# Performance work log

Measured on AMD Instinct MI355X. Metric: run time of the kernel, lower is better.

The kernel has to match this reference:

```python
import jax, jax.numpy as jnp
import numpy as np

N_HEAD = 8
N_FEAT = 512
D_HEAD = N_FEAT // N_HEAD


def setup_inputs() -> dict:
    key = jax.random.key(0)
    ks = jax.random.split(key, 11)
    B, T, L = 4, 2048, 16
    s = 1.0 / np.sqrt(D_HEAD)
    so = 1.0 / np.sqrt(N_FEAT)
    return {
        "q": jax.random.normal(ks[0], (B, T, 1, N_FEAT), jnp.float32),
        "k": jax.random.normal(ks[1], (B, T, L, N_FEAT), jnp.float32),
        "v": jax.random.normal(ks[2], (B, T, L, N_FEAT), jnp.float32),
        "Wq": jax.random.uniform(ks[3], (D_HEAD, D_HEAD), jnp.float32, -s, s),
        "bq": jax.random.uniform(ks[4], (D_HEAD,), jnp.float32, -s, s),
        "Wk": jax.random.uniform(ks[5], (D_HEAD, D_HEAD), jnp.float32, -s, s),
        "bk": jax.random.uniform(ks[6], (D_HEAD,), jnp.float32, -s, s),
        "Wv": jax.random.uniform(ks[7], (D_HEAD, D_HEAD), jnp.float32, -s, s),
        "bv": jax.random.uniform(ks[8], (D_HEAD,), jnp.float32, -s, s),
        "Wo": jax.random.uniform(ks[9], (N_FEAT, N_FEAT), jnp.float32, -so, so),
        "bo": jax.random.uniform(ks[10], (N_FEAT,), jnp.float32, -so, so),
    }


def reference(q, k, v, Wq, bq, Wk, bk, Wv, bv, Wo, bo):
    B, T, L, F = k.shape
    H, D = N_HEAD, D_HEAD
    # split heads: q [B,T,H,D] (query axis of length 1 squeezed), k/v [B,T,L,H,D]
    qh = q.reshape(B, T, H, D)
    kh = k.reshape(B, T, L, H, D)
    vh = v.reshape(B, T, L, H, D)
    # per-head linear projections (shared across heads), Linear: x @ W^T + b
    qh = jnp.einsum("bthd,ed->bthe", qh, Wq) + bq
    kh = jnp.einsum("btlhd,ed->btlhe", kh, Wk) + bk
    vh = jnp.einsum("btlhd,ed->btlhe", vh, Wv) + bv
    # attention scores over the local window L (query length 1 per timestep)
    attw = jnp.einsum("bthd,btlhd->bthl", qh, kh) / jnp.sqrt(jnp.asarray(D, qh.dtype))
    attn = jax.nn.softmax(attw, axis=-1)  # dropout is identity in eval mode
    ct = jnp.einsum("bthl,btlhd->bthd", attn, vh)
    ct = ct.reshape(B, T, F)
    return ct @ Wo.T + bo
```

## Files before the change

### kernel.cpp

```cpp
#include <hip/hip_runtime.h>


#define NFEAT 512
#define NHEAD 8
#define DHEAD 64
#define LWIN  16
#define WPOS  8
#define NBT   4

typedef __attribute__((ext_vector_type(8))) short bf16x8;
typedef __attribute__((ext_vector_type(4))) float f32x4;

__device__ __forceinline__ unsigned short f2bf(float f) {
    unsigned int u = __float_as_uint(f);
    unsigned int r = (u + 0x7fffu + ((u >> 16) & 1u)) >> 16;
    return (unsigned short)r;
}

__global__ void precompute_small(const float* __restrict__ Wq, const float* __restrict__ bq,
                                 const float* __restrict__ Wk,
                                 const float* __restrict__ Wo, const float* __restrict__ bo,
                                 const float* __restrict__ bv,
                                 float* __restrict__ A, float* __restrict__ g,
                                 float* __restrict__ b2) {
    int idx = blockIdx.x * 256 + threadIdx.x;
    if (idx < 4096) {
        int d = idx >> 6, dp = idx & 63;
        float s = 0.f;
        #pragma unroll 8
        for (int e = 0; e < 64; ++e) s = fmaf(Wq[e * 64 + d], Wk[e * 64 + dp], s);
        A[idx] = s;
    } else if (idx < 4160) {
        int dp = idx - 4096;
        float s = 0.f;
        #pragma unroll 8
        for (int e = 0; e < 64; ++e) s = fmaf(Wk[e * 64 + dp], bq[e], s);
        g[dp] = s;
    } else if (idx < 4672) {
        int j = idx - 4160;
        float s = bo[j];
        #pragma unroll 8
        for (int i = 0; i < 512; ++i) s = fmaf(Wo[j * 512 + i], bv[i & 63], s);
        b2[j] = s;
    }
}

__global__ void precompute_wo2(const float* __restrict__ Wo, const float* __restrict__ Wv,
                               unsigned short* __restrict__ Wo2B) {
    int idx = blockIdx.x * 256 + threadIdx.x;
    int i = idx & 511, j = idx >> 9;
    int h = i >> 6, e = i & 63;
    float s = 0.f;
    #pragma unroll 8
    for (int d = 0; d < 64; ++d)
        s = fmaf(Wo[j * 512 + h * 64 + d], Wv[d * 64 + e], s);
    Wo2B[(size_t)j * 512 + i] = f2bf(s);
}

__global__ __launch_bounds__(512, 4)
void w_prepass(const float* __restrict__ q, const float* __restrict__ A,
               const float* __restrict__ g, float* __restrict__ Wm) {
    __shared__ float As[4096];
    __shared__ float qs[WPOS][NFEAT];
    const int tid = threadIdx.x;
    const int bt0 = blockIdx.x * WPOS;

    #pragma unroll
    for (int i = 0; i < 8; ++i) As[i * 512 + tid] = A[i * 512 + tid];
    #pragma unroll
    for (int r = 0; r < WPOS; ++r) qs[r][tid] = q[(size_t)(bt0 + r) * NFEAT + tid];
    __syncthreads();

    const int e  = tid & 63;
    const int hb = (tid >> 6) << 6;
    float acc[WPOS];
    const float ge = g[e];
    #pragma unroll
    for (int r = 0; r < WPOS; ++r) acc[r] = ge;

    #pragma unroll 4
    for (int dq = 0; dq < 16; ++dq) {
        const float a0 = As[(4 * dq + 0) * 64 + e];
        const float a1 = As[(4 * dq + 1) * 64 + e];
        const float a2 = As[(4 * dq + 2) * 64 + e];
        const float a3 = As[(4 * dq + 3) * 64 + e];
        #pragma unroll
        for (int r = 0; r < WPOS; ++r) {
            const float4 qv = *reinterpret_cast<const float4*>(&qs[r][hb + 4 * dq]);
            acc[r] = fmaf(qv.x, a0, acc[r]);
            acc[r] = fmaf(qv.y, a1, acc[r]);
            acc[r] = fmaf(qv.z, a2, acc[r]);
            acc[r] = fmaf(qv.w, a3, acc[r]);
        }
    }
    #pragma unroll
    for (int r = 0; r < WPOS; ++r)
        Wm[(size_t)(bt0 + r) * NFEAT + tid] = acc[r] * 0.125f;
}

__global__ __launch_bounds__(512, 4)
void attn_kv(const float* __restrict__ Wm, const float* __restrict__ k,
             const float* __restrict__ v, unsigned short* __restrict__ vbarBF) {
    __shared__ float ps[NHEAD][NBT][17];

    const int tid = threadIdx.x;
    const int bt0 = blockIdx.x * NBT;

    {
        const int h    = tid >> 6;
        const int lane = tid & 63;
        const int l    = lane >> 2;
        const int d4   = lane & 3;
        #pragma unroll
        for (int pp = 0; pp < NBT; ++pp) {
            const int bt = bt0 + pp;
            const float4* w4 = reinterpret_cast<const float4*>(
                Wm + (size_t)bt * NFEAT + h * 64 + d4 * 16);
            const float4* k4 = reinterpret_cast<const float4*>(
                k + (size_t)bt * (LWIN * NFEAT) + (size_t)l * NFEAT + h * 64 + d4 * 16);
            float a0 = 0.f, a1 = 0.f, a2 = 0.f, a3 = 0.f;
            #pragma unroll
            for (int i = 0; i < 4; ++i) {
                const float4 wq = w4[i];
                const float4 kq = k4[i];
                a0 = fmaf(wq.x, kq.x, a0);
                a1 = fmaf(wq.y, kq.y, a1);
                a2 = fmaf(wq.z, kq.z, a2);
                a3 = fmaf(wq.w, kq.w, a3);
            }
            float sc = (a0 + a1) + (a2 + a3);
            sc += __shfl_xor(sc, 1, 64);
            sc += __shfl_xor(sc, 2, 64);
            const float e = __expf(sc);
            float s = e;
            s += __shfl_xor(s, 4, 64);
            s += __shfl_xor(s, 8, 64);
            s += __shfl_xor(s, 16, 64);
            s += __shfl_xor(s, 32, 64);
            if (d4 == 0) ps[h][pp][l] = e * (1.0f / s);
        }
    }
    __syncthreads();

    {
        const int pp = tid >> 7;
        const int f4 = tid & 127;
        const int h  = f4 >> 4;
        const int bt = bt0 + pp;

        float pv[LWIN];
        #pragma unroll
        for (int i = 0; i < LWIN; ++i) pv[i] = ps[h][pp][i];

        const float4* vp = reinterpret_cast<const float4*>(
            v + (size_t)bt * (LWIN * NFEAT)) + f4;
        float ax = 0.f, ay = 0.f, az = 0.f, aw = 0.f;
        #pragma unroll
        for (int l = 0; l < LWIN; ++l) {
            const float4 vv = vp[(size_t)l * 128];
            ax = fmaf(pv[l], vv.x, ax);
            ay = fmaf(pv[l], vv.y, ay);
            az = fmaf(pv[l], vv.z, az);
            aw = fmaf(pv[l], vv.w, aw);
        }
        unsigned short o[4] = { f2bf(ax), f2bf(ay), f2bf(az), f2bf(aw) };
        *reinterpret_cast<uint2*>(vbarBF + (size_t)bt * NFEAT + f4 * 4) =
            *reinterpret_cast<uint2*>(o);
    }
}

__global__ __launch_bounds__(512, 4)
void out_gemm(const unsigned short* __restrict__ vbarBF,
              const unsigned short* __restrict__ Wo2B,
              const float* __restrict__ b2, float* __restrict__ out) {
    const int tid  = threadIdx.x;
    const int w    = tid >> 6;
    const int lane = tid & 63;
    const int mt   = blockIdx.x;
    const int n0   = w * 64;
    const int r    = lane & 15;
    const int kg   = lane >> 4;

    const short* Ab  = (const short*)vbarBF + ((size_t)(mt * 16 + r)) * 512 + kg * 8;
    const short* Bb0 = (const short*)Wo2B + ((size_t)(n0 +  0 + r)) * 512 + kg * 8;
    const short* Bb1 = (const short*)Wo2B + ((size_t)(n0 + 16 + r)) * 512 + kg * 8;
    const short* Bb2 = (const short*)Wo2B + ((size_t)(n0 + 32 + r)) * 512 + kg * 8;
    const short* Bb3 = (const short*)Wo2B + ((size_t)(n0 + 48 + r)) * 512 + kg * 8;

    f32x4 acc0 = {0.f, 0.f, 0.f, 0.f}, acc1 = acc0, acc2 = acc0, acc3 = acc0;

    #pragma unroll 4
    for (int kk = 0; kk < 16; ++kk) {
        const bf16x8 a   = *reinterpret_cast<const bf16x8*>(Ab  + kk * 32);
        const bf16x8 b0  = *reinterpret_cast<const bf16x8*>(Bb0 + kk * 32);
        const bf16x8 b1  = *reinterpret_cast<const bf16x8*>(Bb1 + kk * 32);
        const bf16x8 b2v = *reinterpret_cast<const bf16x8*>(Bb2 + kk * 32);
        const bf16x8 b3  = *reinterpret_cast<const bf16x8*>(Bb3 + kk * 32);
        acc0 = __builtin_amdgcn_mfma_f32_16x16x32_bf16(a, b0,  acc0, 0, 0, 0);
        acc1 = __builtin_amdgcn_mfma_f32_16x16x32_bf16(a, b1,  acc1, 0, 0, 0);
        acc2 = __builtin_amdgcn_mfma_f32_16x16x32_bf16(a, b2v, acc2, 0, 0, 0);
        acc3 = __builtin_amdgcn_mfma_f32_16x16x32_bf16(a, b3,  acc3, 0, 0, 0);
    }

    const float bb0 = b2[n0 + 0 + r],  bb1 = b2[n0 + 16 + r];
    const float bb2 = b2[n0 + 32 + r], bb3 = b2[n0 + 48 + r];
    #pragma unroll
    for (int j = 0; j < 4; ++j) {
        const size_t row = (size_t)(mt * 16 + kg * 4 + j) * 512;
        out[row + n0 +  0 + r] = acc0[j] + bb0;
        out[row + n0 + 16 + r] = acc1[j] + bb1;
        out[row + n0 + 32 + r] = acc2[j] + bb2;
        out[row + n0 + 48 + r] = acc3[j] + bb3;
    }
}

extern "C" void kernel_launch(void* const* d_in, const int* in_sizes, int n_in,
                              void* d_out, int out_size, void* d_ws, size_t ws_size,
                              hipStream_t stream) {
    const float* q  = (const float*)d_in[0];
    const float* k  = (const float*)d_in[1];
    const float* v  = (const float*)d_in[2];
    const float* Wq = (const float*)d_in[3];
    const float* bq = (const float*)d_in[4];
    const float* Wk = (const float*)d_in[5];
    const float* Wv = (const float*)d_in[7];
    const float* bv = (const float*)d_in[8];
    const float* Wo = (const float*)d_in[9];
    const float* bo = (const float*)d_in[10];
    float* out = (float*)d_out;

    float* ws = (float*)d_ws;
    float*          A      = ws;
    float*          g      = ws + 4096;
    float*          b2     = ws + 4160;
    unsigned short* Wo2B   = (unsigned short*)(ws + 4672);
    float*          Wm     = ws + 4672 + 131072;
    unsigned short* vbarBF = (unsigned short*)(ws + 4672 + 131072 + 4194304);

    const int BT = in_sizes[0] / NFEAT;

    hipLaunchKernelGGL(precompute_small, dim3(19), dim3(256), 0, stream,
                       Wq, bq, Wk, Wo, bo, bv, A, g, b2);
    hipLaunchKernelGGL(precompute_wo2, dim3(1024), dim3(256), 0, stream,
                       Wo, Wv, Wo2B);
    hipLaunchKernelGGL(w_prepass, dim3(BT / WPOS), dim3(512), 0, stream,
                       q, A, g, Wm);
    hipLaunchKernelGGL(attn_kv, dim3(BT / NBT), dim3(512), 0, stream,
                       Wm, k, v, vbarBF);
    hipLaunchKernelGGL(out_gemm, dim3(BT / 16), dim3(512), 0, stream,
                       vbarBF, Wo2B, b2, out);
}
```

Measured before the change: 196.5 us.

## Fuse attention-over-window and output GEMM into one kernel via shared memory

Merges the attn_kv and out_gemm kernels into one kernel that handles 16 timesteps per block. The per-timestep query projections are staged in LDS, and the bf16 attention outputs stay in padded LDS rather than round-tripping through global memory before the MFMA output projection. This removes one launch and the vbar write/read traffic. In exchange it uses more LDS per block, issues a quarter as many blocks for the streaming k/v phase, and adds another block-wide barrier.

```diff
diff --git a/kernel.cpp b/kernel.cpp
--- a/kernel.cpp
+++ b/kernel.cpp
@@ -6,7 +6,8 @@
 #define DHEAD 64
 #define LWIN  16
 #define WPOS  8
-#define NBT   4
+#define FBT   16
+#define VPITCH 520
 
 typedef __attribute__((ext_vector_type(8))) short bf16x8;
 typedef __attribute__((ext_vector_type(4))) float f32x4;
@@ -99,25 +100,33 @@
 }
 
 __global__ __launch_bounds__(512, 4)
-void attn_kv(const float* __restrict__ Wm, const float* __restrict__ k,
-             const float* __restrict__ v, unsigned short* __restrict__ vbarBF) {
-    __shared__ float ps[NHEAD][NBT][17];
+void attn_fused(const float* __restrict__ Wm, const float* __restrict__ k,
+                const float* __restrict__ v, const unsigned short* __restrict__ Wo2B,
+                const float* __restrict__ b2, float* __restrict__ out) {
+    __shared__ float ps[NHEAD][FBT][17];
+    __shared__ __align__(16) unsigned char uni[FBT * NFEAT * 4];
+    float*          wsT   = reinterpret_cast<float*>(uni);
+    unsigned short* vbarS = reinterpret_cast<unsigned short*>(uni);
 
     const int tid = threadIdx.x;
-    const int bt0 = blockIdx.x * NBT;
+    const int bt0 = blockIdx.x * FBT;
+
+    #pragma unroll 4
+    for (int r = 0; r < FBT; ++r)
+        wsT[r * NFEAT + tid] = Wm[(size_t)(bt0 + r) * NFEAT + tid];
+    __syncthreads();
 
     {
         const int h    = tid >> 6;
         const int lane = tid & 63;
         const int l    = lane >> 2;
         const int d4   = lane & 3;
-        #pragma unroll
-        for (int pp = 0; pp < NBT; ++pp) {
-            const int bt = bt0 + pp;
+        #pragma unroll 4
+        for (int pp = 0; pp < FBT; ++pp) {
             const float4* w4 = reinterpret_cast<const float4*>(
-                Wm + (size_t)bt * NFEAT + h * 64 + d4 * 16);
+                wsT + pp * NFEAT + h * 64 + d4 * 16);
             const float4* k4 = reinterpret_cast<const float4*>(
-                k + (size_t)bt * (LWIN * NFEAT) + (size_t)l * NFEAT + h * 64 + d4 * 16);
+                k + (size_t)(bt0 + pp) * (LWIN * NFEAT) + (size_t)l * NFEAT + h * 64 + d4 * 16);
             float a0 = 0.f, a1 = 0.f, a2 = 0.f, a3 = 0.f;
             #pragma unroll
             for (int i = 0; i < 4; ++i) {
@@ -143,74 +152,71 @@
     __syncthreads();
 
     {
-        const int pp = tid >> 7;
+        const int pb = tid >> 7;
         const int f4 = tid & 127;
-        const int h  = f4 >> 4;
-        const int bt = bt0 + pp;
-
-        float pv[LWIN];
+        const int hh = f4 >> 4;
         #pragma unroll
-        for (int i = 0; i < LWIN; ++i) pv[i] = ps[h][pp][i];
-
-        const float4* vp = reinterpret_cast<const float4*>(
-            v + (size_t)bt * (LWIN * NFEAT)) + f4;
-        float ax = 0.f, ay = 0.f, az = 0.f, aw = 0.f;
+        for (int ii = 0; ii < 4; ++ii) {
+            const int bt = ii * 4 + pb;
+            float pv[LWIN];
+            #pragma unroll
+            for (int i = 0; i < LWIN; ++i) pv[i] = ps[hh][bt][i];
+            const float4* vp = reinterpret_cast<const float4*>(
+                v + (size_t)(bt0 + bt) * (LWIN * NFEAT)) + f4;
+            float ax = 0.f, ay = 0.f, az = 0.f, aw = 0.f;
+            #pragma unroll
+            for (int l = 0; l < LWIN; ++l) {
+                const float4 vv = vp[(size_t)l * 128];
+                ax = fmaf(pv[l], vv.x, ax);
+                ay = fmaf(pv[l], vv.y, ay);
+                az = fmaf(pv[l], vv.z, az);
+                aw = fmaf(pv[l], vv.w, aw);
+            }
+            unsigned short o[4] = { f2bf(ax), f2bf(ay), f2bf(az), f2bf(aw) };
+            *reinterpret_cast<uint2*>(vbarS + bt * VPITCH + f4 * 4) =
+                *reinterpret_cast<uint2*>(o);
+        }
+    }
+    __syncthreads();
+
+    {
+        const int w    = tid >> 6;
+        const int lane = tid & 63;
+        const int n0   = w * 64;
+        const int r    = lane & 15;
+        const int kg   = lane >> 4;
+
+        const unsigned short* As0 = vbarS + r * VPITCH + kg * 8;
+        const short* Bb0 = (const short*)Wo2B + ((size_t)(n0 +  0 + r)) * 512 + kg * 8;
+        const short* Bb1 = (const short*)Wo2B + ((size_t)(n0 + 16 + r)) * 512 + kg * 8;
+        const short* Bb2 = (const short*)Wo2B + ((size_t)(n0 + 32 + r)) * 512 + kg * 8;
+        const short* Bb3 = (const short*)Wo2B + ((size_t)(n0 + 48 + r)) * 512 + kg * 8;
+
+        f32x4 acc0 = {0.f, 0.f, 0.f, 0.f}, acc1 = acc0, acc2 = acc0, acc3 = acc0;
+
+        #pragma unroll 4
+        for (int kk = 0; kk < 16; ++kk) {
+            const bf16x8 a   = *reinterpret_cast<const bf16x8*>(As0 + kk * 32);
+            const bf16x8 b0  = *reinterpret_cast<const bf16x8*>(Bb0 + kk * 32);
+            const bf16x8 b1  = *reinterpret_cast<const bf16x8*>(Bb1 + kk * 32);
+            const bf16x8 b2v = *reinterpret_cast<const bf16x8*>(Bb2 + kk * 32);
+            const bf16x8 b3  = *reinterpret_cast<const bf16x8*>(Bb3 + kk * 32);
+            acc0 = __builtin_amdgcn_mfma_f32_16x16x32_bf16(a, b0,  acc0, 0, 0, 0);
+            acc1 = __builtin_amdgcn_mfma_f32_16x16x32_bf16(a, b1,  acc1, 0, 0, 0);
+            acc2 = __builtin_amdgcn_mfma_f32_16x16x32_bf16(a, b2v, acc2, 0, 0, 0);
+            acc3 = __builtin_amdgcn_mfma_f32_16x16x32_bf16(a, b3,  acc3, 0, 0, 0);
+        }
+
+        const float bb0 = b2[n0 + 0 + r],  bb1 = b2[n0 + 16 + r];
+        const float bb2 = b2[n0 + 32 + r], bb3 = b2[n0 + 48 + r];
         #pragma unroll
-        for (int l = 0; l < LWIN; ++l) {
-            const float4 vv = vp[(size_t)l * 128];
-            ax = fmaf(pv[l], vv.x, ax);
-            ay = fmaf(pv[l], vv.y, ay);
-            az = fmaf(pv[l], vv.z, az);
-            aw = fmaf(pv[l], vv.w, aw);
-        }
-        unsigned short o[4] = { f2bf(ax), f2bf(ay), f2bf(az), f2bf(aw) };
-        *reinterpret_cast<uint2*>(vbarBF + (size_t)bt * NFEAT + f4 * 4) =
-            *reinterpret_cast<uint2*>(o);
-    }
-}
-
-__global__ __launch_bounds__(512, 4)
-void out_gemm(const unsigned short* __restrict__ vbarBF,
-              const unsigned short* __restrict__ Wo2B,
-              const float* __restrict__ b2, float* __restrict__ out) {
-    const int tid  = threadIdx.x;
-    const int w    = tid >> 6;
-    const int lane = tid & 63;
-    const int mt   = blockIdx.x;
-    const int n0   = w * 64;
-    const int r    = lane & 15;
-    const int kg   = lane >> 4;
-
-    const short* Ab  = (const short*)vbarBF + ((size_t)(mt * 16 + r)) * 512 + kg * 8;
-    const short* Bb0 = (const short*)Wo2B + ((size_t)(n0 +  0 + r)) * 512 + kg * 8;
-    const short* Bb1 = (const short*)Wo2B + ((size_t)(n0 + 16 + r)) * 512 + kg * 8;
-    const short* Bb2 = (const short*)Wo2B + ((size_t)(n0 + 32 + r)) * 512 + kg * 8;
-    const short* Bb3 = (const short*)Wo2B + ((size_t)(n0 + 48 + r)) * 512 + kg * 8;
-
-    f32x4 acc0 = {0.f, 0.f, 0.f, 0.f}, acc1 = acc0, acc2 = acc0, acc3 = acc0;
-
-    #pragma unroll 4
-    for (int kk = 0; kk < 16; ++kk) {
-        const bf16x8 a   = *reinterpret_cast<const bf16x8*>(Ab  + kk * 32);
-        const bf16x8 b0  = *reinterpret_cast<const bf16x8*>(Bb0 + kk * 32);
-        const bf16x8 b1  = *reinterpret_cast<const bf16x8*>(Bb1 + kk * 32);
-        const bf16x8 b2v = *reinterpret_cast<const bf16x8*>(Bb2 + kk * 32);
-        const bf16x8 b3  = *reinterpret_cast<const bf16x8*>(Bb3 + kk * 32);
-        acc0 = __builtin_amdgcn_mfma_f32_16x16x32_bf16(a, b0,  acc0, 0, 0, 0);
-        acc1 = __builtin_amdgcn_mfma_f32_16x16x32_bf16(a, b1,  acc1, 0, 0, 0);
-        acc2 = __builtin_amdgcn_mfma_f32_16x16x32_bf16(a, b2v, acc2, 0, 0, 0);
-        acc3 = __builtin_amdgcn_mfma_f32_16x16x32_bf16(a, b3,  acc3, 0, 0, 0);
-    }
-
-    const float bb0 = b2[n0 + 0 + r],  bb1 = b2[n0 + 16 + r];
-    const float bb2 = b2[n0 + 32 + r], bb3 = b2[n0 + 48 + r];
-    #pragma unroll
-    for (int j = 0; j < 4; ++j) {
-        const size_t row = (size_t)(mt * 16 + kg * 4 + j) * 512;
-        out[row + n0 +  0 + r] = acc0[j] + bb0;
-        out[row + n0 + 16 + r] = acc1[j] + bb1;
-        out[row + n0 + 32 + r] = acc2[j] + bb2;
-        out[row + n0 + 48 + r] = acc3[j] + bb3;
+        for (int j = 0; j < 4; ++j) {
+            const size_t row = (size_t)(bt0 + kg * 4 + j) * 512;
+            out[row + n0 +  0 + r] = acc0[j] + bb0;
+            out[row + n0 + 16 + r] = acc1[j] + bb1;
+            out[row + n0 + 32 + r] = acc2[j] + bb2;
+            out[row + n0 + 48 + r] = acc3[j] + bb3;
+        }
     }
 }
 
@@ -230,12 +236,11 @@
     float* out = (float*)d_out;
 
     float* ws = (float*)d_ws;
-    float*          A      = ws;
-    float*          g      = ws + 4096;
-    float*          b2     = ws + 4160;
-    unsigned short* Wo2B   = (unsigned short*)(ws + 4672);
-    float*          Wm     = ws + 4672 + 131072;
-    unsigned short* vbarBF = (unsigned short*)(ws + 4672 + 131072 + 4194304);
+    float*          A    = ws;
+    float*          g    = ws + 4096;
+    float*          b2   = ws + 4160;
+    unsigned short* Wo2B = (unsigned short*)(ws + 4672);
+    float*          Wm   = ws + 4672 + 131072;
 
     const int BT = in_sizes[0] / NFEAT;
 
@@ -245,8 +250,6 @@
                        Wo, Wv, Wo2B);
     hipLaunchKernelGGL(w_prepass, dim3(BT / WPOS), dim3(512), 0, stream,
                        q, A, g, Wm);
-    hipLaunchKernelGGL(attn_kv, dim3(BT / NBT), dim3(512), 0, stream,
-                       Wm, k, v, vbarBF);
-    hipLaunchKernelGGL(out_gemm, dim3(BT / 16), dim3(512), 0, stream,
-                       vbarBF, Wo2B, b2, out);
-}
+    hipLaunchKernelGGL(attn_fused, dim3(BT / FBT), dim3(512), 0, stream,
+                       Wm, k, v, Wo2B, b2, out);
+}
```

Result: faster. 174.9 us (-11.0%).

## Stream K/V through double-buffered LDS with async global-to-LDS loads

Applied to the files above, without the earlier changes.

Replaces the attention kernel with a streaming kernel in which each block walks 32 consecutive timesteps. The K and V windows for the next timestep are prefetched into a double-buffered LDS area using direct global-to-LDS loads, with an XOR swizzle on K to avoid bank conflicts. The Wm rows are prefetched into registers one step ahead. Softmax is fused with the V reduction through wave shuffles, which removes the intermediate probability buffer. The aim is to overlap memory latency with compute. The cost is far fewer blocks, about 128KB of LDS per block, and a block-wide barrier every timestep, which may limit how many bytes are in flight.

```diff
diff --git a/kernel.cpp b/kernel.cpp
--- a/kernel.cpp
+++ b/kernel.cpp
@@ -6,7 +6,7 @@
 #define DHEAD 64
 #define LWIN  16
 #define WPOS  8
-#define NBT   4
+#define NBT   32
 
 typedef __attribute__((ext_vector_type(8))) short bf16x8;
 typedef __attribute__((ext_vector_type(4))) float f32x4;
@@ -15,6 +15,12 @@
     unsigned int u = __float_as_uint(f);
     unsigned int r = (u + 0x7fffu + ((u >> 16) & 1u)) >> 16;
     return (unsigned short)r;
+}
+
+__device__ __forceinline__ void gload16(const float* src, float* dst) {
+    __builtin_amdgcn_global_load_lds((const __attribute__((address_space(1))) float*)src,
+                                     (__attribute__((address_space(3))) float*)dst,
+                                     16, 0, 0);
 }
 
 __global__ void precompute_small(const float* __restrict__ Wq, const float* __restrict__ bq,
@@ -98,75 +104,107 @@
         Wm[(size_t)(bt0 + r) * NFEAT + tid] = acc[r] * 0.125f;
 }
 
-__global__ __launch_bounds__(512, 4)
-void attn_kv(const float* __restrict__ Wm, const float* __restrict__ k,
-             const float* __restrict__ v, unsigned short* __restrict__ vbarBF) {
-    __shared__ float ps[NHEAD][NBT][17];
-
-    const int tid = threadIdx.x;
-    const int bt0 = blockIdx.x * NBT;
-
+__global__ __launch_bounds__(512, 2)
+void attn_stream(const float* __restrict__ Wm, const float* __restrict__ k,
+                 const float* __restrict__ v, unsigned short* __restrict__ vbarG,
+                 int BT) {
+    __shared__ __align__(16) float kbuf[2][LWIN][NFEAT];
+    __shared__ __align__(16) float vbuf[2][LWIN][NFEAT];
+
+    const int tid  = threadIdx.x;
+    const int w    = tid >> 6;
+    const int lane = tid & 63;
+    const int lq   = lane >> 2;
+    const int d4   = lane & 3;
+    const int bt0  = blockIdx.x * NBT;
+
+    const int wmoff = w * 64 + d4 * 16;
+    float4 wmc0, wmc1, wmc2, wmc3, wmn0, wmn1, wmn2, wmn3;
     {
-        const int h    = tid >> 6;
-        const int lane = tid & 63;
-        const int l    = lane >> 2;
-        const int d4   = lane & 3;
+        const float* p = Wm + (size_t)bt0 * NFEAT + wmoff;
+        wmc0 = *(const float4*)(p + 0);
+        wmc1 = *(const float4*)(p + 4);
+        wmc2 = *(const float4*)(p + 8);
+        wmc3 = *(const float4*)(p + 12);
+    }
+
+    {
+        const float* kb = k + (size_t)bt0 * (LWIN * NFEAT);
+        const float* vb = v + (size_t)bt0 * (LWIN * NFEAT);
         #pragma unroll
-        for (int pp = 0; pp < NBT; ++pp) {
-            const int bt = bt0 + pp;
-            const float4* w4 = reinterpret_cast<const float4*>(
-                Wm + (size_t)bt * NFEAT + h * 64 + d4 * 16);
-            const float4* k4 = reinterpret_cast<const float4*>(
-                k + (size_t)bt * (LWIN * NFEAT) + (size_t)l * NFEAT + h * 64 + d4 * 16);
-            float a0 = 0.f, a1 = 0.f, a2 = 0.f, a3 = 0.f;
+        for (int rr = 0; rr < 2; ++rr) {
+            const int r    = 2 * w + rr;
+            const int kofs = ((lane * 16) ^ ((r & 7) << 4)) >> 2;
+            gload16(kb + r * NFEAT +       kofs,     &kbuf[0][r][0]);
+            gload16(kb + r * NFEAT + 256 + kofs,     &kbuf[0][r][256]);
+            gload16(vb + r * NFEAT +       lane * 4, &vbuf[0][r][0]);
+            gload16(vb + r * NFEAT + 256 + lane * 4, &vbuf[0][r][256]);
+        }
+    }
+    __syncthreads();
+
+    const int half  = (w >> 2) & 1;
+    const int hwoff = (w & 3) * 256 + d4 * 64;
+    const int swz   = (lq & 7) << 4;
+
+    for (int i = 0; i < NBT; ++i) {
+        const int cur = i & 1;
+        const int bt  = bt0 + i;
+
+        if (i + 1 < NBT) {
+            const float* kb = k + (size_t)(bt + 1) * (LWIN * NFEAT);
+            const float* vb = v + (size_t)(bt + 1) * (LWIN * NFEAT);
+            const int nb = cur ^ 1;
             #pragma unroll
-            for (int i = 0; i < 4; ++i) {
-                const float4 wq = w4[i];
-                const float4 kq = k4[i];
-                a0 = fmaf(wq.x, kq.x, a0);
-                a1 = fmaf(wq.y, kq.y, a1);
-                a2 = fmaf(wq.z, kq.z, a2);
-                a3 = fmaf(wq.w, kq.w, a3);
+            for (int rr = 0; rr < 2; ++rr) {
+                const int r    = 2 * w + rr;
+                const int kofs = ((lane * 16) ^ ((r & 7) << 4)) >> 2;
+                gload16(kb + r * NFEAT +       kofs,     &kbuf[nb][r][0]);
+                gload16(kb + r * NFEAT + 256 + kofs,     &kbuf[nb][r][256]);
+                gload16(vb + r * NFEAT +       lane * 4, &vbuf[nb][r][0]);
+                gload16(vb + r * NFEAT + 256 + lane * 4, &vbuf[nb][r][256]);
             }
-            float sc = (a0 + a1) + (a2 + a3);
-            sc += __shfl_xor(sc, 1, 64);
-            sc += __shfl_xor(sc, 2, 64);
-            const float e = __expf(sc);
-            float s = e;
-            s += __shfl_xor(s, 4, 64);
-            s += __shfl_xor(s, 8, 64);
-            s += __shfl_xor(s, 16, 64);
-            s += __shfl_xor(s, 32, 64);
-            if (d4 == 0) ps[h][pp][l] = e * (1.0f / s);
-        }
-    }
-    __syncthreads();
-
-    {
-        const int pp = tid >> 7;
-        const int f4 = tid & 127;
-        const int h  = f4 >> 4;
-        const int bt = bt0 + pp;
-
-        float pv[LWIN];
-        #pragma unroll
-        for (int i = 0; i < LWIN; ++i) pv[i] = ps[h][pp][i];
-
-        const float4* vp = reinterpret_cast<const float4*>(
-            v + (size_t)bt * (LWIN * NFEAT)) + f4;
-        float ax = 0.f, ay = 0.f, az = 0.f, aw = 0.f;
+        }
+        {
+            const int btn = (i + 1 < NBT) ? bt + 1 : bt;
+            const float* p = Wm + (size_t)btn * NFEAT + wmoff;
+            wmn0 = *(const float4*)(p + 0);
+            wmn1 = *(const float4*)(p + 4);
+            wmn2 = *(const float4*)(p + 8);
+            wmn3 = *(const float4*)(p + 12);
+        }
+        __builtin_amdgcn_sched_barrier(0);
+
+        const char* rowb = (const char*)&kbuf[cur][lq][0] + half * 1024;
+        const float4 k0 = *(const float4*)(rowb + ((hwoff +  0) ^ swz));
+        const float4 k1 = *(const float4*)(rowb + ((hwoff + 16) ^ swz));
+        const float4 k2 = *(const float4*)(rowb + ((hwoff + 32) ^ swz));
+        const float4 k3 = *(const float4*)(rowb + ((hwoff + 48) ^ swz));
+        float s0 = wmc0.x * k0.x, s1 = wmc1.x * k1.x, s2 = wmc2.x * k2.x, s3 = wmc3.x * k3.x;
+        s0 = fmaf(wmc0.y, k0.y, s0); s1 = fmaf(wmc1.y, k1.y, s1);
+        s2 = fmaf(wmc2.y, k2.y, s2); s3 = fmaf(wmc3.y, k3.y, s3);
+        s0 = fmaf(wmc0.z, k0.z, s0); s1 = fmaf(wmc1.z, k1.z, s1);
+        s2 = fmaf(wmc2.z, k2.z, s2); s3 = fmaf(wmc3.z, k3.z, s3);
+        s0 = fmaf(wmc0.w, k0.w, s0); s1 = fmaf(wmc1.w, k1.w, s1);
+        s2 = fmaf(wmc2.w, k2.w, s2); s3 = fmaf(wmc3.w, k3.w, s3);
+        float s = (s0 + s1) + (s2 + s3);
+        s += __shfl_xor(s, 1, 64);
+        s += __shfl_xor(s, 2, 64);
+        const float e = __expf(s);
+
+        float den = 0.f, acc = 0.f;
         #pragma unroll
         for (int l = 0; l < LWIN; ++l) {
-            const float4 vv = vp[(size_t)l * 128];
-            ax = fmaf(pv[l], vv.x, ax);
-            ay = fmaf(pv[l], vv.y, ay);
-            az = fmaf(pv[l], vv.z, az);
-            aw = fmaf(pv[l], vv.w, aw);
-        }
-        unsigned short o[4] = { f2bf(ax), f2bf(ay), f2bf(az), f2bf(aw) };
-        *reinterpret_cast<uint2*>(vbarBF + (size_t)bt * NFEAT + f4 * 4) =
-            *reinterpret_cast<uint2*>(o);
-    }
+            const float el = __shfl(e, 4 * l, 64);
+            den += el;
+            acc = fmaf(el, vbuf[cur][l][w * 64 + lane], acc);
+        }
+        vbarG[(size_t)bt * NFEAT + tid] = f2bf(acc * (1.0f / den));
+
+        wmc0 = wmn0; wmc1 = wmn1; wmc2 = wmn2; wmc3 = wmn3;
+        __syncthreads();
+    }
+    (void)BT;
 }
 
 __global__ __launch_bounds__(512, 4)
@@ -235,7 +273,7 @@
     float*          b2     = ws + 4160;
     unsigned short* Wo2B   = (unsigned short*)(ws + 4672);
     float*          Wm     = ws + 4672 + 131072;
-    unsigned short* vbarBF = (unsigned short*)(ws + 4672 + 131072 + 4194304);
+    unsigned short* vbarG  = (unsigned short*)(ws + 4672 + 131072 + 4194304);
 
     const int BT = in_sizes[0] / NFEAT;
 
@@ -245,8 +283,8 @@
                        Wo, Wv, Wo2B);
     hipLaunchKernelGGL(w_prepass, dim3(BT / WPOS), dim3(512), 0, stream,
                        q, A, g, Wm);
-    hipLaunchKernelGGL(attn_kv, dim3(BT / NBT), dim3(512), 0, stream,
-                       Wm, k, v, vbarBF);
+    hipLaunchKernelGGL(attn_stream, dim3(BT / NBT), dim3(512), 0, stream,
+                       Wm, k, v, vbarG, BT);
     hipLaunchKernelGGL(out_gemm, dim3(BT / 16), dim3(512), 0, stream,
-                       vbarBF, Wo2B, b2, out);
-}
+                       vbarG, Wo2B, b2, out);
+}
```

New measurement: 211.4 us. 1.08x slower.
